# Performance work log

Measured on AMD Instinct MI355X. Metric: run time of the kernel, lower is better.

Reference implementation:

```python
import jax, jax.numpy as jnp
import numpy as np

B, S, IN, H = 16, 512, 512, 256
TAU_TRACE = 20.0
TAU_MEM = 20.0
DECAY_TRACE = float(np.exp(-1.0 / TAU_TRACE))  # exp_convolve decay
DECAY_MEM = float(np.exp(-1.0 / TAU_MEM))      # leaky-integrator dynamics decay
LR = 0.01                                       # plasticity learning rate
W_MAX = 1.0                                     # soft upper bound on fast weights


def setup_inputs() -> dict:
    key = jax.random.key(0)
    k1, k2 = jax.random.split(key)
    x = jax.random.normal(k1, (B, S, IN), dtype=jnp.float32)
    # xavier_uniform with gain=sqrt(2) on W of shape [2H, IN]
    lim = float(np.sqrt(2.0) * np.sqrt(6.0 / (2 * H + IN)))
    W = jax.random.uniform(k2, (2 * H, IN), dtype=jnp.float32, minval=-lim, maxval=lim)
    return {"x": x, "W": W}


def reference(x, W):
    # i = x @ W^T : [B, S, 2H], then split into key/value input currents
    i = jnp.einsum('bsi,hi->bsh', x, W)
    ik, iv = jnp.split(i, 2, axis=2)  # each [B, S, H]
    bsz = x.shape[0]
    h = W.shape[0] // 2

    def step(carry, inp):
        kv, vv, kt, vt, mem = carry
        ik_t, iv_t = inp  # [B, H] each
        # key dynamics (leaky integrator + tanh)
        kv = DECAY_MEM * kv + ik_t
        key = jnp.tanh(kv)
        # memory readout: 0.2 * (key.unsqueeze(1) * mem).sum(2) == 0.2 * mem @ key
        ikv = 0.2 * jnp.einsum('bij,bj->bi', mem, key)
        # value dynamics
        vv = DECAY_MEM * vv + iv_t + ikv
        val = jnp.tanh(vv)
        # exponential traces
        kt = DECAY_TRACE * kt + (1.0 - DECAY_TRACE) * key
        vt = DECAY_TRACE * vt + (1.0 - DECAY_TRACE) * val
        # soft-bounded Hebbian outer-product fast-weight update
        mem = mem + LR * (vt[:, :, None] * kt[:, None, :]) * (W_MAX - mem)
        return (kv, vv, kt, vt, mem), (key, val)

    z = jnp.zeros((bsz, h), x.dtype)
    mem0 = jnp.zeros((bsz, h, h), x.dtype)
    (_, _, _, _, mem), (keys, vals) = jax.lax.scan(
        step, (z, z, z, z, mem0),
        (jnp.swapaxes(ik, 0, 1), jnp.swapaxes(iv, 0, 1)))  # scan over time
    return mem, jnp.swapaxes(keys, 0, 1), jnp.swapaxes(vals, 0, 1)
```

## Files before the change

### kernel.cpp

```cpp
#include <hip/hip_runtime.h>

#define BB 16
#define SS 512
#define KIN 512
#define H 256

typedef float v2f __attribute__((ext_vector_type(2)));

constexpr float DECAY   = 0.951229424500714f;
constexpr float OMD     = 0.048770575499286f;
constexpr float DECAY64 = 0.040762203978366f;
constexpr float LR      = 0.01f;

__device__ __forceinline__ float fast_tanh(float x) {
    float e = __expf(2.f * x);
    return 1.f - __fdividef(2.f, e + 1.f);
}

__device__ __forceinline__ v2f pk_mul(v2f a, v2f b) {
    v2f d; asm("v_pk_mul_f32 %0, %1, %2" : "=v"(d) : "v"(a), "v"(b)); return d;
}
__device__ __forceinline__ v2f pk_fma(v2f a, v2f b, v2f c) {
    v2f d; asm("v_pk_fma_f32 %0, %1, %2, %3" : "=v"(d) : "v"(a), "v"(b), "v"(c)); return d;
}

__device__ __forceinline__ void allred32x2(float x, float y, float& rx, float& ry) {
    int t, u;
    t = __builtin_amdgcn_update_dpp(0, __float_as_int(x), 0x111, 0xf, 0xf, false);
    u = __builtin_amdgcn_update_dpp(0, __float_as_int(y), 0x111, 0xf, 0xf, false);
    x += __int_as_float(t); y += __int_as_float(u);
    t = __builtin_amdgcn_update_dpp(0, __float_as_int(x), 0x112, 0xf, 0xf, false);
    u = __builtin_amdgcn_update_dpp(0, __float_as_int(y), 0x112, 0xf, 0xf, false);
    x += __int_as_float(t); y += __int_as_float(u);
    t = __builtin_amdgcn_update_dpp(0, __float_as_int(x), 0x114, 0xf, 0xf, false);
    u = __builtin_amdgcn_update_dpp(0, __float_as_int(y), 0x114, 0xf, 0xf, false);
    x += __int_as_float(t); y += __int_as_float(u);
    t = __builtin_amdgcn_update_dpp(0, __float_as_int(x), 0x118, 0xf, 0xf, false);
    u = __builtin_amdgcn_update_dpp(0, __float_as_int(y), 0x118, 0xf, 0xf, false);
    x += __int_as_float(t); y += __int_as_float(u);
    t = __builtin_amdgcn_update_dpp(0, __float_as_int(x), 0x142, 0xa, 0xf, false);
    u = __builtin_amdgcn_update_dpp(0, __float_as_int(y), 0x142, 0xa, 0xf, false);
    x += __int_as_float(t); y += __int_as_float(u);
    rx = __int_as_float(__builtin_amdgcn_ds_swizzle(__float_as_int(x), 0x3E0));
    ry = __int_as_float(__builtin_amdgcn_ds_swizzle(__float_as_int(y), 0x3E0));
}

__global__ __launch_bounds__(256) void gemm_xwT(const float* __restrict__ X,
                                                const float* __restrict__ W,
                                                float* __restrict__ ik_out,
                                                float* __restrict__ iv_t) {
    __shared__ float As[2][16][68];
    __shared__ float Bs[2][16][68];
    const int m0 = blockIdx.y * 64;
    const int n0 = blockIdx.x * 64;
    const int tid = threadIdx.x;
    const int r  = tid >> 2;
    const int cg = tid & 3;
    const int tx = tid & 15;
    const int ty = tid >> 4;

    const float* xp = &X[(size_t)(m0 + r) * KIN + cg * 4];
    const float* wp = &W[(size_t)(n0 + r) * KIN + cg * 4];

    float acc[4][4] = {};
    float4 av = *(const float4*)(xp);
    float4 bv = *(const float4*)(wp);
    As[0][cg*4+0][r] = av.x; As[0][cg*4+1][r] = av.y; As[0][cg*4+2][r] = av.z; As[0][cg*4+3][r] = av.w;
    Bs[0][cg*4+0][r] = bv.x; Bs[0][cg*4+1][r] = bv.y; Bs[0][cg*4+2][r] = bv.z; Bs[0][cg*4+3][r] = bv.w;
    __syncthreads();

    int cur = 0;
    for (int c = 0; c < KIN / 16; ++c) {
        if (c + 1 < KIN / 16) {
            av = *(const float4*)(xp + (size_t)(c + 1) * 16);
            bv = *(const float4*)(wp + (size_t)(c + 1) * 16);
        }
#pragma unroll
        for (int kk = 0; kk < 16; ++kk) {
            float4 a = *(const float4*)&As[cur][kk][ty * 4];
            float4 b = *(const float4*)&Bs[cur][kk][tx * 4];
            float ar[4] = {a.x, a.y, a.z, a.w};
            float br[4] = {b.x, b.y, b.z, b.w};
#pragma unroll
            for (int i = 0; i < 4; ++i)
#pragma unroll
                for (int j = 0; j < 4; ++j) acc[i][j] += ar[i] * br[j];
        }
        if (c + 1 < KIN / 16) {
            const int nb = cur ^ 1;
            As[nb][cg*4+0][r] = av.x; As[nb][cg*4+1][r] = av.y;
            As[nb][cg*4+2][r] = av.z; As[nb][cg*4+3][r] = av.w;
            Bs[nb][cg*4+0][r] = bv.x; Bs[nb][cg*4+1][r] = bv.y;
            Bs[nb][cg*4+2][r] = bv.z; Bs[nb][cg*4+3][r] = bv.w;
            __syncthreads();
            cur = nb;
        }
    }

    if (n0 < 256) {
#pragma unroll
        for (int i = 0; i < 4; ++i) {
            float4 o = make_float4(acc[i][0], acc[i][1], acc[i][2], acc[i][3]);
            *(float4*)&ik_out[(size_t)(m0 + ty * 4 + i) * 256 + n0 + tx * 4] = o;
        }
    } else {
        const int b  = m0 >> 9;
        const int s0 = (m0 & 511) + ty * 4;
#pragma unroll
        for (int j = 0; j < 4; ++j) {
            float4 o = make_float4(acc[0][j], acc[1][j], acc[2][j], acc[3][j]);
            *(float4*)&iv_t[((size_t)b * H + (n0 - 256 + tx * 4 + j)) * SS + s0] = o;
        }
    }
}


__global__ __launch_bounds__(256) void ks1_chunk(const float* __restrict__ ik,
                                                 float* __restrict__ E) {
    const int tid  = blockIdx.x * 256 + threadIdx.x;
    const int col  = tid & 255;
    const int rest = tid >> 8;
    const int b    = rest >> 3;
    const int ch   = rest & 7;
    const float* p = ik + ((size_t)(b * SS + ch * 64)) * 256 + col;
    float e = 0.f;
    float rb[4];
#pragma unroll
    for (int j = 0; j < 4; ++j) rb[j] = p[(size_t)j * 256];
    for (int j0 = 0; j0 < 64; j0 += 4) {
#pragma unroll
        for (int j = 0; j < 4; ++j) {
            float v = rb[j];
            int jn = j0 + 4 + j; if (jn > 63) jn = 63;
            rb[j] = p[(size_t)jn * 256];
            e = __builtin_fmaf(DECAY, e, v);
        }
    }
    E[((size_t)b * 8 + ch) * 256 + col] = e;
}

__global__ __launch_bounds__(64) void ks2_carry(const float* __restrict__ E,
                                                float* __restrict__ Sst) {
    const int idx = blockIdx.x * 64 + threadIdx.x;
    const int b   = idx >> 8;
    const int col = idx & 255;
    float carry = 0.f;
#pragma unroll
    for (int c = 0; c < 8; ++c) {
        Sst[((size_t)b * 8 + c) * 256 + col] = carry;
        carry = __builtin_fmaf(DECAY64, carry, E[((size_t)b * 8 + c) * 256 + col]);
    }
}

__global__ __launch_bounds__(256) void ks3_emit(const float* __restrict__ ik,
                                                const float* __restrict__ Sst,
                                                float* __restrict__ keys) {
    const int tid  = blockIdx.x * 256 + threadIdx.x;
    const int col  = tid & 255;
    const int rest = tid >> 8;
    const int b    = rest >> 3;
    const int ch   = rest & 7;
    const float* p = ik + ((size_t)(b * SS + ch * 64)) * 256 + col;
    float* ko = keys + ((size_t)(b * SS + ch * 64)) * H + col;
    float kv = Sst[((size_t)b * 8 + ch) * 256 + col];
    float rb[4];
#pragma unroll
    for (int j = 0; j < 4; ++j) rb[j] = p[(size_t)j * 256];
    for (int j0 = 0; j0 < 64; j0 += 4) {
#pragma unroll
        for (int j = 0; j < 4; ++j) {
            float v = rb[j];
            int jn = j0 + 4 + j; if (jn > 63) jn = 63;
            rb[j] = p[(size_t)jn * 256];
            kv = __builtin_fmaf(DECAY, kv, v);
            ko[(size_t)(j0 + j) * H] = fast_tanh(kv);
        }
    }
}

__global__ __launch_bounds__(256, 2) void value_scan(const float* __restrict__ keys,
                                                     const float* __restrict__ iv_t,
                                                     float* __restrict__ mem_out,
                                                     float* __restrict__ vals) {
    const int tid  = threadIdx.x;
    const int wave = tid >> 6;
    const int lane = tid & 63;
    const int sub  = lane & 31;
    const int half = lane >> 5;
    const int b    = blockIdx.x & 15;
    const int rg   = blockIdx.x >> 4;
    const int row  = rg * 8 + wave * 2 + half;
    const int so   = sub * 8;

    const float* kp  = keys + (size_t)b * SS * H + so;
    const float* ivp = iv_t + ((size_t)b * H + row) * SS;
    float* vrow = vals + (size_t)b * SS * H + row;

    const v2f DEC2 = {DECAY, DECAY};
    const v2f OMD2 = {OMD, OMD};

    v2f nm0 = {0.f,0.f}, nm1 = {0.f,0.f}, nm2 = {0.f,0.f}, nm3 = {0.f,0.f};
    v2f w0  = {0.f,0.f}, w1  = {0.f,0.f}, w2  = {0.f,0.f}, w3  = {0.f,0.f};
    v2f kt0 = {0.f,0.f}, kt1 = {0.f,0.f}, kt2 = {0.f,0.f}, kt3 = {0.f,0.f};
    float vv = 0.f, vt = 0.f, c = 0.f, ar = 0.f, br = 0.f, stash = 0.f;

    v2f kp0 = *(const v2f*)(kp + 0), kp1 = *(const v2f*)(kp + 2),
        kp2 = *(const v2f*)(kp + 4), kp3 = *(const v2f*)(kp + 6);
    v2f kR[4][4];
#pragma unroll
    for (int j = 0; j < 4; ++j)
#pragma unroll
        for (int q = 0; q < 4; ++q)
            kR[j][q] = *(const v2f*)(kp + (size_t)(1 + j) * H + q * 2);
    const float* kpF = kp + 5 * H;

    float4 iA0 = *(const float4*)(ivp + 0);
    float4 iA1 = *(const float4*)(ivp + 4);
    float4 iB0 = *(const float4*)(ivp + 8);
    float4 iB1 = *(const float4*)(ivp + 12);
    ivp += 16;

#define VS_STEP(J, RELK)                                                       \
    {                                                                          \
        v2f kc0 = kR[(J)&3][0], kc1 = kR[(J)&3][1],                            \
            kc2 = kR[(J)&3][2], kc3 = kR[(J)&3][3];                            \
        if (RELK) {                                                            \
            kR[(J)&3][0] = *(const v2f*)(kpF + ((J)&3) * H + 0);               \
            kR[(J)&3][1] = *(const v2f*)(kpF + ((J)&3) * H + 2);               \
            kR[(J)&3][2] = *(const v2f*)(kpF + ((J)&3) * H + 4);               \
            kR[(J)&3][3] = *(const v2f*)(kpF + ((J)&3) * H + 6);               \
        }                                                                      \
        v2f nc2 = {-c, -c};                                                    \
        nm0 = pk_fma(nc2, w0, nm0);                                            \
        nm1 = pk_fma(nc2, w1, nm1);                                            \
        nm2 = pk_fma(nc2, w2, nm2);                                            \
        nm3 = pk_fma(nc2, w3, nm3);                                            \
        kt0 = pk_fma(DEC2, kt0, pk_mul(OMD2, kp0));                            \
        kt1 = pk_fma(DEC2, kt1, pk_mul(OMD2, kp1));                            \
        kt2 = pk_fma(DEC2, kt2, pk_mul(OMD2, kp2));                            \
        kt3 = pk_fma(DEC2, kt3, pk_mul(OMD2, kp3));                            \
        w0 = pk_fma(kt0, nm0, kt0);                                            \
        w1 = pk_fma(kt1, nm1, kt1);                                            \
        w2 = pk_fma(kt2, nm2, kt2);                                            \
        w3 = pk_fma(kt3, nm3, kt3);                                            \
        v2f a2 = pk_mul(nm0, kc0);                                             \
        a2 = pk_fma(nm1, kc1, a2);                                             \
        a2 = pk_fma(nm2, kc2, a2);                                             \
        a2 = pk_fma(nm3, kc3, a2);                                             \
        v2f b2 = pk_mul(w0, kc0);                                              \
        b2 = pk_fma(w1, kc1, b2);                                              \
        b2 = pk_fma(w2, kc2, b2);                                              \
        b2 = pk_fma(w3, kc3, b2);                                              \
        float ra, rb2;                                                         \
        allred32x2(a2.x + a2.y, b2.x + b2.y, ra, rb2);                         \
        float arn = -0.2f * ra;                                                \
        float brn =  0.2f * rb2;                                               \
        kp0 = kc0; kp1 = kc1; kp2 = kc2; kp3 = kc3;                            \
        float vvt = __builtin_fmaf(DECAY, vv, ivs[J]) + ar;                    \
        vv = __builtin_fmaf(c, br, vvt);                                       \
        float valv = fast_tanh(vv);                                            \
        vt = __builtin_fmaf(DECAY, vt, OMD * valv);                            \
        if (sub == (J)) stash = valv;                                          \
        c = LR * vt;                                                           \
        ar = arn; br = brn;                                                    \
        asm volatile("" ::: "memory");                                         \
    }

    for (int t0 = 0; t0 < SS - 16; t0 += 16) {
        float4 nA0 = *(const float4*)(ivp + 0);
        float4 nA1 = *(const float4*)(ivp + 4);
        float4 nB0 = *(const float4*)(ivp + 8);
        float4 nB1 = *(const float4*)(ivp + 12);
        ivp += 16;
        {
            float ivs[16] = {iA0.x, iA0.y, iA0.z, iA0.w,
                             iA1.x, iA1.y, iA1.z, iA1.w,
                             iB0.x, iB0.y, iB0.z, iB0.w,
                             iB1.x, iB1.y, iB1.z, iB1.w};
            VS_STEP(0, 1)  VS_STEP(1, 1)  VS_STEP(2, 1)  VS_STEP(3, 1)
            kpF += 4 * H;
            VS_STEP(4, 1)  VS_STEP(5, 1)  VS_STEP(6, 1)  VS_STEP(7, 1)
            kpF += 4 * H;
            VS_STEP(8, 1)  VS_STEP(9, 1)  VS_STEP(10, 1) VS_STEP(11, 1)
            kpF += 4 * H;
            VS_STEP(12, 1) VS_STEP(13, 1) VS_STEP(14, 1) VS_STEP(15, 1)
            kpF += 4 * H;
        }
        if (sub < 16) vrow[(size_t)sub * H] = stash;
        vrow += 16 * H;
        iA0 = nA0; iA1 = nA1; iB0 = nB0; iB1 = nB1;
    }
    {
        float ivs[16] = {iA0.x, iA0.y, iA0.z, iA0.w,
                         iA1.x, iA1.y, iA1.z, iA1.w,
                         iB0.x, iB0.y, iB0.z, iB0.w,
                         iB1.x, iB1.y, iB1.z, iB1.w};
        VS_STEP(0, 1)  VS_STEP(1, 1)  VS_STEP(2, 1)  VS_STEP(3, 1)
        kpF += 4 * H;
        VS_STEP(4, 1)  VS_STEP(5, 1)  VS_STEP(6, 1)  VS_STEP(7, 1)
        kpF += 4 * H;
        VS_STEP(8, 1)  VS_STEP(9, 1)  VS_STEP(10, 1) VS_STEP(11, 0)
        VS_STEP(12, 0) VS_STEP(13, 0) VS_STEP(14, 0) VS_STEP(15, 0)
        if (sub < 16) vrow[(size_t)sub * H] = stash;
    }
#undef VS_STEP

    {
        v2f ncf = {-c, -c};
        nm0 = pk_fma(ncf, w0, nm0);
        nm1 = pk_fma(ncf, w1, nm1);
        nm2 = pk_fma(ncf, w2, nm2);
        nm3 = pk_fma(ncf, w3, nm3);
    }
    float* mo = &mem_out[((size_t)b * H + row) * H + so];
    *(float4*)&mo[0] = make_float4(-nm0.x, -nm0.y, -nm1.x, -nm1.y);
    *(float4*)&mo[4] = make_float4(-nm2.x, -nm2.y, -nm3.x, -nm3.y);
}

extern "C" void kernel_launch(void* const* d_in, const int* in_sizes, int n_in,
                              void* d_out, int out_size, void* d_ws, size_t ws_size,
                              hipStream_t stream) {
    const float* x = (const float*)d_in[0];
    const float* W = (const float*)d_in[1];
    float* out = (float*)d_out;
    float* mem_out = out;
    float* keys = out + (size_t)BB * H * H;
    float* vals = keys + (size_t)BB * SS * H;
    float* ik   = (float*)d_ws;
    float* iv_t = ik + (size_t)BB * SS * 256;
    float* E    = vals;
    float* Sst  = vals + 32768;

    dim3 gb(8, 128);
    gemm_xwT<<<gb, 256, 0, stream>>>(x, W, ik, iv_t);
    ks1_chunk<<<128, 256, 0, stream>>>(ik, E);
    ks2_carry<<<64, 64, 0, stream>>>(E, Sst);
    ks3_emit<<<128, 256, 0, stream>>>(ik, Sst, keys);
    value_scan<<<512, 256, 0, stream>>>(keys, iv_t, mem_out, vals);
}
```

Before: 240.3 us.

## Split key scan into 64 chunks of 8 and fold OMD scaling into LR

The three-phase key recurrence scan now uses 64 chunks of 8 timesteps instead of 8 chunks of 64. This gives 1024 blocks rather than 128 for the chunk and emit kernels, exposing more parallelism and shortening each thread's serial dependency chain. In exchange the carry kernel runs a longer 64-step serial chain per column. In the value scan, the (1-decay) factor on the key trace is dropped and folded into the learning-rate constant, which removes a packed multiply per step.

Measured after the change: 227.3 us. 1.06x faster.

```diff
diff --git a/kernel.cpp b/kernel.cpp
--- a/kernel.cpp
+++ b/kernel.cpp
@@ -7,10 +7,11 @@
 
 typedef float v2f __attribute__((ext_vector_type(2)));
 
-constexpr float DECAY   = 0.951229424500714f;
-constexpr float OMD     = 0.048770575499286f;
-constexpr float DECAY64 = 0.040762203978366f;
-constexpr float LR      = 0.01f;
+constexpr float DECAY  = 0.951229424500714f;
+constexpr float OMD    = 0.048770575499286f;
+constexpr float DECAY8 = 0.670320046035639f;
+constexpr float LR     = 0.01f;
+constexpr float CLO    = 4.8770575499286e-4f;
 
 __device__ __forceinline__ float fast_tanh(float x) {
     float e = __expf(2.f * x);
@@ -117,26 +118,17 @@
 
 __global__ __launch_bounds__(256) void ks1_chunk(const float* __restrict__ ik,
                                                  float* __restrict__ E) {
-    const int tid  = blockIdx.x * 256 + threadIdx.x;
-    const int col  = tid & 255;
-    const int rest = tid >> 8;
-    const int b    = rest >> 3;
-    const int ch   = rest & 7;
-    const float* p = ik + ((size_t)(b * SS + ch * 64)) * 256 + col;
+    const int col = threadIdx.x;
+    const int b   = blockIdx.x >> 6;
+    const int ch  = blockIdx.x & 63;
+    const float* p = ik + ((size_t)(b * SS + ch * 8)) * 256 + col;
+    float rb[8];
+#pragma unroll
+    for (int j = 0; j < 8; ++j) rb[j] = p[(size_t)j * 256];
     float e = 0.f;
-    float rb[4];
-#pragma unroll
-    for (int j = 0; j < 4; ++j) rb[j] = p[(size_t)j * 256];
-    for (int j0 = 0; j0 < 64; j0 += 4) {
-#pragma unroll
-        for (int j = 0; j < 4; ++j) {
-            float v = rb[j];
-            int jn = j0 + 4 + j; if (jn > 63) jn = 63;
-            rb[j] = p[(size_t)jn * 256];
-            e = __builtin_fmaf(DECAY, e, v);
-        }
-    }
-    E[((size_t)b * 8 + ch) * 256 + col] = e;
+#pragma unroll
+    for (int j = 0; j < 8; ++j) e = __builtin_fmaf(DECAY, e, rb[j]);
+    E[((size_t)b * 64 + ch) * 256 + col] = e;
 }
 
 __global__ __launch_bounds__(64) void ks2_carry(const float* __restrict__ E,
@@ -144,37 +136,35 @@
     const int idx = blockIdx.x * 64 + threadIdx.x;
     const int b   = idx >> 8;
     const int col = idx & 255;
+    const float* Eb = E + (size_t)b * 64 * 256 + col;
+    float* Sb = Sst + (size_t)b * 64 * 256 + col;
+    float eb[64];
+#pragma unroll
+    for (int c = 0; c < 64; ++c) eb[c] = Eb[(size_t)c * 256];
     float carry = 0.f;
 #pragma unroll
-    for (int c = 0; c < 8; ++c) {
-        Sst[((size_t)b * 8 + c) * 256 + col] = carry;
-        carry = __builtin_fmaf(DECAY64, carry, E[((size_t)b * 8 + c) * 256 + col]);
+    for (int c = 0; c < 64; ++c) {
+        Sb[(size_t)c * 256] = carry;
+        carry = __builtin_fmaf(DECAY8, carry, eb[c]);
     }
 }
 
 __global__ __launch_bounds__(256) void ks3_emit(const float* __restrict__ ik,
                                                 const float* __restrict__ Sst,
                                                 float* __restrict__ keys) {
-    const int tid  = blockIdx.x * 256 + threadIdx.x;
-    const int col  = tid & 255;
-    const int rest = tid >> 8;
-    const int b    = rest >> 3;
-    const int ch   = rest & 7;
-    const float* p = ik + ((size_t)(b * SS + ch * 64)) * 256 + col;
-    float* ko = keys + ((size_t)(b * SS + ch * 64)) * H + col;
-    float kv = Sst[((size_t)b * 8 + ch) * 256 + col];
-    float rb[4];
-#pragma unroll
-    for (int j = 0; j < 4; ++j) rb[j] = p[(size_t)j * 256];
-    for (int j0 = 0; j0 < 64; j0 += 4) {
-#pragma unroll
-        for (int j = 0; j < 4; ++j) {
-            float v = rb[j];
-            int jn = j0 + 4 + j; if (jn > 63) jn = 63;
-            rb[j] = p[(size_t)jn * 256];
-            kv = __builtin_fmaf(DECAY, kv, v);
-            ko[(size_t)(j0 + j) * H] = fast_tanh(kv);
-        }
+    const int col = threadIdx.x;
+    const int b   = blockIdx.x >> 6;
+    const int ch  = blockIdx.x & 63;
+    const float* p = ik + ((size_t)(b * SS + ch * 8)) * 256 + col;
+    float* ko = keys + ((size_t)(b * SS + ch * 8)) * H + col;
+    float rb[8];
+#pragma unroll
+    for (int j = 0; j < 8; ++j) rb[j] = p[(size_t)j * 256];
+    float kv = Sst[((size_t)b * 64 + ch) * 256 + col];
+#pragma unroll
+    for (int j = 0; j < 8; ++j) {
+        kv = __builtin_fmaf(DECAY, kv, rb[j]);
+        ko[(size_t)j * H] = fast_tanh(kv);
     }
 }
 
@@ -197,7 +187,6 @@
     float* vrow = vals + (size_t)b * SS * H + row;
 
     const v2f DEC2 = {DECAY, DECAY};
-    const v2f OMD2 = {OMD, OMD};
 
     v2f nm0 = {0.f,0.f}, nm1 = {0.f,0.f}, nm2 = {0.f,0.f}, nm3 = {0.f,0.f};
     v2f w0  = {0.f,0.f}, w1  = {0.f,0.f}, w2  = {0.f,0.f}, w3  = {0.f,0.f};
@@ -235,10 +224,10 @@
         nm1 = pk_fma(nc2, w1, nm1);                                            \
         nm2 = pk_fma(nc2, w2, nm2);                                            \
         nm3 = pk_fma(nc2, w3, nm3);                                            \
-        kt0 = pk_fma(DEC2, kt0, pk_mul(OMD2, kp0));                            \
-        kt1 = pk_fma(DEC2, kt1, pk_mul(OMD2, kp1));                            \
-        kt2 = pk_fma(DEC2, kt2, pk_mul(OMD2, kp2));                            \
-        kt3 = pk_fma(DEC2, kt3, pk_mul(OMD2, kp3));                            \
+        kt0 = pk_fma(DEC2, kt0, kp0);                                          \
+        kt1 = pk_fma(DEC2, kt1, kp1);                                          \
+        kt2 = pk_fma(DEC2, kt2, kp2);                                          \
+        kt3 = pk_fma(DEC2, kt3, kp3);                                          \
         w0 = pk_fma(kt0, nm0, kt0);                                            \
         w1 = pk_fma(kt1, nm1, kt1);                                            \
         w2 = pk_fma(kt2, nm2, kt2);                                            \
@@ -261,7 +250,7 @@
         float valv = fast_tanh(vv);                                            \
         vt = __builtin_fmaf(DECAY, vt, OMD * valv);                            \
         if (sub == (J)) stash = valv;                                          \
-        c = LR * vt;                                                           \
+        c = CLO * vt;                                                          \
         ar = arn; br = brn;                                                    \
         asm volatile("" ::: "memory");                                         \
     }
@@ -329,12 +318,12 @@
     float* ik   = (float*)d_ws;
     float* iv_t = ik + (size_t)BB * SS * 256;
     float* E    = vals;
-    float* Sst  = vals + 32768;
+    float* Sst  = vals + 262144;
 
     dim3 gb(8, 128);
     gemm_xwT<<<gb, 256, 0, stream>>>(x, W, ik, iv_t);
-    ks1_chunk<<<128, 256, 0, stream>>>(ik, E);
+    ks1_chunk<<<1024, 256, 0, stream>>>(ik, E);
     ks2_carry<<<64, 64, 0, stream>>>(E, Sst);
-    ks3_emit<<<128, 256, 0, stream>>>(ik, Sst, keys);
+    ks3_emit<<<1024, 256, 0, stream>>>(ik, Sst, keys);
     value_scan<<<512, 256, 0, stream>>>(keys, iv_t, mem_out, vals);
 }
```
